# Kernel optimization log

Measured on AMD Instinct MI355X. Metric: run time of the kernel, lower is better.

The kernel has to match this reference:

```python
import jax, jax.numpy as jnp
import numpy as np

H, HID, VD, NB = 8, 128, 16, 4
EN_LOC, DE_LOC = 5.0, 5.0
FMAX = jnp.float32(3.4028235e38)

def _gelu(x):
    return jax.nn.gelu(x, approximate=False)  # keras gelu default = erf form

def _mlp(x, W1, b1, W2, b2):
    return _gelu(x @ W1 + b1) @ W2 + b2

def _mhpa(m_dist, x, r, w, locality):
    # m_dist: (B,N,N), r: (1,H,1,1), w: (H,HID,VD)
    sd = m_dist[:, None, :, :] * (r ** 2)  # (B,H,N,N)
    if locality <= 100:
        n = sd.shape[-1]
        pos = locality / 100.0 * (n - 1)  # tfp linear percentile position
        lo = int(np.floor(pos)); hi = int(np.ceil(pos)); frac = np.float32(pos - lo)
        s = jnp.sort(sd, axis=-1)
        thr = s[..., lo] * (1.0 - frac) + s[..., hi] * frac  # (B,H,N)
        sd = jnp.where(sd <= thr[..., None], sd, FMAX)
    att = jax.nn.softmax(-sd, axis=-1)  # masked entries -> exp(-huge) = 0
    v = jnp.einsum('bnj,hjk->bhnk', x, w)  # (B,H,N,VD)
    o = jnp.einsum('bhnj,bhjd->bhnd', att, v)  # (B,H,N,VD)
    B, Hh, N, D = o.shape
    return _gelu(o.transpose(0, 2, 1, 3).reshape(B, N, Hh * D))

def setup_inputs() -> dict:
    B, N, IN, OUT = 2, 2048, 3, 1
    ks = jax.random.split(jax.random.key(0), 40)
    def dn(k, shape, fan):
        return (jax.random.normal(k, shape) / np.sqrt(fan)).astype(jnp.float32)
    d = {}
    d['m_dist'] = jax.random.uniform(ks[0], (B, N, N), dtype=jnp.float32)
    d['inputs'] = jax.random.normal(ks[1], (B, N, IN), dtype=jnp.float32)
    d['en_W'] = dn(ks[2], (IN, HID), IN); d['en_b'] = jnp.zeros((HID,), jnp.float32)
    d['down_r'] = jax.random.uniform(ks[3], (1, H, 1, 1), dtype=jnp.float32)
    d['down_w'] = dn(ks[4], (H, HID, VD), HID)
    d['mlp1_W1'] = dn(ks[5], (HID, HID), HID); d['mlp1_b1'] = jnp.zeros((HID,), jnp.float32)
    d['mlp1_W2'] = dn(ks[6], (HID, HID), HID); d['mlp1_b2'] = jnp.zeros((HID,), jnp.float32)
    d['w1_W'] = dn(ks[7], (HID, HID), HID); d['w1_b'] = jnp.zeros((HID,), jnp.float32)
    d['pa_r'] = jax.random.uniform(ks[8], (NB, 1, H, 1, 1), dtype=jnp.float32)
    d['pa_w'] = dn(ks[9], (NB, H, HID, VD), HID)
    d['blk_W1'] = dn(ks[10], (NB, HID, HID), HID); d['blk_b1'] = jnp.zeros((NB, HID), jnp.float32)
    d['blk_W2'] = dn(ks[11], (NB, HID, HID), HID); d['blk_b2'] = jnp.zeros((NB, HID), jnp.float32)
    d['wi_W'] = dn(ks[12], (NB, HID, HID), HID); d['wi_b'] = jnp.zeros((NB, HID), jnp.float32)
    d['up_r'] = jax.random.uniform(ks[13], (1, H, 1, 1), dtype=jnp.float32)
    d['up_w'] = dn(ks[14], (H, HID, VD), HID)
    d['mlp2_W1'] = dn(ks[15], (HID, HID), HID); d['mlp2_b1'] = jnp.zeros((HID,), jnp.float32)
    d['mlp2_W2'] = dn(ks[16], (HID, HID), HID); d['mlp2_b2'] = jnp.zeros((HID,), jnp.float32)
    d['w2_W'] = dn(ks[17], (HID, HID), HID); d['w2_b'] = jnp.zeros((HID,), jnp.float32)
    d['de_W1'] = dn(ks[18], (HID, HID), HID); d['de_b1'] = jnp.zeros((HID,), jnp.float32)
    d['de_W2'] = dn(ks[19], (HID, OUT), HID); d['de_b2'] = jnp.zeros((OUT,), jnp.float32)
    return d

def reference(m_dist, inputs, en_W, en_b, down_r, down_w, mlp1_W1, mlp1_b1, mlp1_W2, mlp1_b2,
              w1_W, w1_b, pa_r, pa_w, blk_W1, blk_b1, blk_W2, blk_b2, wi_W, wi_b,
              up_r, up_w, mlp2_W1, mlp2_b1, mlp2_W2, mlp2_b2, w2_W, w2_b,
              de_W1, de_b1, de_W2, de_b2):
    en = _gelu(inputs @ en_W + en_b)
    x = _mlp(_mhpa(m_dist, en, down_r, down_w, EN_LOC), mlp1_W1, mlp1_b1, mlp1_W2, mlp1_b2) + (en @ w1_W + w1_b)
    x = _gelu(x)
    for i in range(NB):
        h = _mhpa(m_dist, x, pa_r[i], pa_w[i], 200)  # locality=200 -> no mask
        x = _gelu(_mlp(h, blk_W1[i], blk_b1[i], blk_W2[i], blk_b2[i]) + (x @ wi_W[i] + wi_b[i]))
    de = _mlp(_mhpa(m_dist, x, up_r, up_w, DE_LOC), mlp2_W1, mlp2_b1, mlp2_W2, mlp2_b2) + (x @ w2_W + w2_b)
    de = _gelu(de)
    return _mlp(de, de_W1, de_b1, de_W2, de_b2)
```

## Files before the change

kernel.cpp:

```cpp
#include <hip/hip_runtime.h>
#include <hip/hip_bf16.h>
#include <cstddef>

#define NROWS 4096
#define HIDD  128
#define NH    8
#define VD    16

typedef __attribute__((ext_vector_type(8))) short bf16x8;
typedef __attribute__((ext_vector_type(4))) float f32x4;
typedef __attribute__((ext_vector_type(4))) unsigned int u32x4;

__device__ __forceinline__ float gelu_f(float x) {
    return 0.5f * x * (1.0f + erff(x * 0.70710678118654752440f));
}

__device__ __forceinline__ unsigned short bf16_rne(float f) {
    union { float f; unsigned u; } x; x.f = f;
    unsigned r = x.u + 0x7FFFu + ((x.u >> 16) & 1u);
    return (unsigned short)(r >> 16);
}
__device__ __forceinline__ float bf16_to_f(unsigned short h) {
    union { unsigned u; float f; } x; x.u = ((unsigned)h) << 16;
    return x.f;
}
__device__ __forceinline__ unsigned pk_bf16(float a, float b) {
    __hip_bfloat162 t = __float22bfloat162_rn(make_float2(a, b));
    unsigned u; __builtin_memcpy(&u, &t, 4); return u;
}

__device__ __forceinline__ void split8(const float* av, bf16x8& hi, bf16x8& lo) {
    #pragma unroll
    for (int j = 0; j < 8; ++j) {
        unsigned short h = bf16_rne(av[j]);
        unsigned short l = bf16_rne(av[j] - bf16_to_f(h));
        hi[j] = (short)h; lo[j] = (short)l;
    }
}

__device__ __forceinline__ void load_a_global(const float* __restrict__ X,
                                              int row0, int lane,
                                              bf16x8* ahi, bf16x8* alo) {
    const int q = lane >> 4, mr = lane & 15;
    const float* xr = X + (size_t)(row0 + mr) * 128 + q * 8;
    #pragma unroll
    for (int kt = 0; kt < 4; ++kt) {
        float av[8];
        *(float4*)(av)     = *(const float4*)(xr + kt * 32);
        *(float4*)(av + 4) = *(const float4*)(xr + kt * 32 + 4);
        split8(av, ahi[kt], alo[kt]);
    }
}
__device__ __forceinline__ void load_a_lds(const float (*xT)[132], int lane,
                                           bf16x8* ahi, bf16x8* alo) {
    const int q = lane >> 4, mr = lane & 15;
    #pragma unroll
    for (int kt = 0; kt < 4; ++kt) {
        float av[8];
        *(float4*)(av)     = *(const float4*)&xT[mr][kt * 32 + q * 8];
        *(float4*)(av + 4) = *(const float4*)&xT[mr][kt * 32 + q * 8 + 4];
        split8(av, ahi[kt], alo[kt]);
    }
}

__device__ __forceinline__ f32x4 mm3(f32x4 acc, bf16x8 ahi, bf16x8 alo,
                                     const unsigned short* __restrict__ bp, int kt) {
    bf16x8 bhi = *(const bf16x8*)(bp + kt * 512);
    bf16x8 blo = *(const bf16x8*)(bp + 16384 + kt * 512);
    acc = __builtin_amdgcn_mfma_f32_16x16x32_bf16(ahi, bhi, acc, 0, 0, 0);
    acc = __builtin_amdgcn_mfma_f32_16x16x32_bf16(ahi, blo, acc, 0, 0, 0);
    acc = __builtin_amdgcn_mfma_f32_16x16x32_bf16(alo, bhi, acc, 0, 0, 0);
    return acc;
}

__device__ __forceinline__ void vproj_lds(const float (*xT)[132], int row0,
                                          const unsigned short* __restrict__ Vw,
                                          unsigned short* __restrict__ vblk) {
    const int tid = threadIdx.x, wave = tid >> 6, lane = tid & 63;
    const int q = lane >> 4, mr = lane & 15;
    bf16x8 ahi[4], alo[4];
    load_a_lds(xT, lane, ahi, alo);
    #pragma unroll
    for (int ct = 0; ct < 2; ++ct) {
        int nt = wave * 2 + ct;
        const unsigned short* bp = Vw + (size_t)nt * 2048 + lane * 8;
        f32x4 acc = (f32x4){0.f, 0.f, 0.f, 0.f};
        #pragma unroll
        for (int kt = 0; kt < 4; ++kt) acc = mm3(acc, ahi[kt], alo[kt], bp, kt);
        int c = nt * 16 + mr;
        int r0 = row0 + q * 4;
        int bb = r0 >> 11, n = r0 & 2047;
        int jt = n >> 5, q2 = (n >> 3) & 3, jj = n & 7;
        int h = c >> 4, dd = c & 15;
        size_t off = (((size_t)(bb * 8 + h) * 64 + jt) * 4 + q2) * 128
                   + (dd << 3) + jj;
        uint2 st = make_uint2(pk_bf16(acc[0], acc[1]), pk_bf16(acc[2], acc[3]));
        *(uint2*)(vblk + off) = st;
    }
}

struct PrepArgs { const float* src[25]; unsigned vwmask; };

__global__ __launch_bounds__(256) void prep_percentile_kernel(
    PrepArgs a, unsigned short* __restrict__ dst,
    const float* __restrict__ m, float* __restrict__ m102, float* __restrict__ m103)
{
    if (blockIdx.x < 100) {
        const int mat = blockIdx.x >> 2, chunk = blockIdx.x & 3;
        const float* __restrict__ W = a.src[mat];
        const int vw = (a.vwmask >> mat) & 1;
        unsigned short* __restrict__ base = dst + (size_t)mat * 32768;
        for (int o = chunk * 4096 + threadIdx.x; o < chunk * 4096 + 4096; o += 256) {
            int nt = o >> 11, kt = (o >> 9) & 3, q = (o >> 7) & 3;
            int n16 = (o >> 3) & 15, jj = o & 7;
            int k = kt * 32 + q * 8 + jj;
            float w = vw ? W[nt * 2048 + k * 16 + n16]
                         : W[k * 128 + nt * 16 + n16];
            unsigned short h = bf16_rne(w);
            unsigned short l = bf16_rne(w - bf16_to_f(h));
            base[o] = h;
            base[16384 + o] = l;
        }
        return;
    }

    __shared__ int   cnt[256];
    __shared__ int   cum[256];
    __shared__ float buf[192];
    __shared__ int   nc;
    __shared__ int   sb0, sb1, sbase;

    const int row = blockIdx.x - 100;
    const int t   = threadIdx.x;
    const float* mr = m + (size_t)row * 2048;

    float4 aa = *(const float4*)(mr + t * 8);
    float4 cc = *(const float4*)(mr + t * 8 + 4);
    float v[8] = {aa.x, aa.y, aa.z, aa.w, cc.x, cc.y, cc.z, cc.w};

    cnt[t] = 0;
    if (t == 0) nc = 0;
    __syncthreads();

    int bidx[8];
    #pragma unroll
    for (int i = 0; i < 8; ++i) {
        int bi = (int)(v[i] * 256.0f);
        bi = bi < 0 ? 0 : (bi > 255 ? 255 : bi);
        bidx[i] = bi;
        atomicAdd(&cnt[bi], 1);
    }
    __syncthreads();

    if (t < 64) {
        int c0 = cnt[t * 4], c1 = cnt[t * 4 + 1], c2 = cnt[t * 4 + 2], c3 = cnt[t * 4 + 3];
        int s1 = c0 + c1, s2 = s1 + c2, s3 = s2 + c3;
        int sc = s3;
        #pragma unroll
        for (int off = 1; off < 64; off <<= 1) {
            int o = __shfl_up(sc, off);
            if (t >= off) sc += o;
        }
        int base = sc - s3;
        cum[t * 4]     = base + c0;
        cum[t * 4 + 1] = base + s1;
        cum[t * 4 + 2] = base + s2;
        cum[t * 4 + 3] = base + s3;
    }
    __syncthreads();

    {
        int cprev = (t == 0) ? 0 : cum[t - 1];
        int cthis = cum[t];
        if (cprev < 103 && 103 <= cthis) { sb0 = t; sbase = cprev; }
        if (cprev < 104 && 104 <= cthis) { sb1 = t; }
    }
    __syncthreads();

    const int b0 = sb0, b1 = sb1, base = sbase;
    #pragma unroll
    for (int i = 0; i < 8; ++i) {
        if (bidx[i] >= b0 && bidx[i] <= b1) {
            int p = atomicAdd(&nc, 1);
            if (p < 192) buf[p] = v[i];
        }
    }
    __syncthreads();

    int n = nc; if (n > 192) n = 192;
    if (t < n) {
        float x = buf[t];
        int rk = base;
        for (int j = 0; j < n; ++j) {
            float y = buf[j];
            rk += (y < x || (y == x && j < t)) ? 1 : 0;
        }
        if (rk == 102) m102[row] = x;
        if (rk == 103) m103[row] = x;
    }
}

__global__ __launch_bounds__(256) void encoder_vproj_kernel(
    const float* __restrict__ inp, const float* __restrict__ W,
    const float* __restrict__ b, float* __restrict__ ben,
    const unsigned short* __restrict__ Vw, unsigned short* __restrict__ vblk)
{
    __shared__ float xT[16][132];
    const int tid = threadIdx.x;
    const int row0 = blockIdx.x * 16;
    const int ri = tid >> 4, c0 = (tid & 15) * 8;
    const int row = row0 + ri;
    float x0 = inp[row * 3], x1 = inp[row * 3 + 1], x2 = inp[row * 3 + 2];
    float o[8];
    #pragma unroll
    for (int j = 0; j < 8; ++j) {
        int c = c0 + j;
        o[j] = gelu_f(x0 * W[c] + x1 * W[128 + c] + x2 * W[256 + c] + b[c]);
        xT[ri][c0 + j] = o[j];
    }
    *(float4*)(ben + (size_t)row * 128 + c0)     = *(float4*)(o);
    *(float4*)(ben + (size_t)row * 128 + c0 + 4) = *(float4*)(o + 4);
    __syncthreads();
    vproj_lds(xT, row0, Vw, vblk);
}

__global__ __launch_bounds__(512) void attn_mlp_kernel(
    const float* __restrict__ m_dist,
    const unsigned short* __restrict__ vblk,
    const float* __restrict__ rvec,
    const float* __restrict__ m102, const float* __restrict__ m103,
    const unsigned short* __restrict__ W1b, const float* __restrict__ b1,
    float* __restrict__ bt, int masked)
{
    __shared__ float partLDS[4][16][128];
    __shared__ float sumLDS[4][8][16];
    __shared__ float bhT[16][132];

    const int tid  = threadIdx.x;
    const int wave = tid >> 6, lane = tid & 63;
    const int hg = wave & 1, jq = wave >> 1;
    const int q = lane >> 4, rn = lane & 15;
    const int row0 = blockIdx.x * 16;
    const int row  = row0 + rn;
    const int b    = row0 >> 11;
    const int n    = row & 2047;

    float r2[4], c2[4], thr[4];
    {
        const double pos = 5.0 / 100.0 * 2047.0;
        const float FRAC = (float)(pos - 102.0);
        const float OM   = 1.0f - FRAC;
        float t102 = m102[row], t103 = m103[row];
        #pragma unroll
        for (int hh = 0; hh < 4; ++hh) {
            float r = rvec[hg * 4 + hh];
            r2[hh] = r * r;
            c2[hh] = -r2[hh] * 1.44269504088896340736f;
            thr[hh] = masked ? ((t102 * r2[hh]) * OM + (t103 * r2[hh]) * FRAC)
                             : 3.4028235e38f;
        }
    }

    const float* mrow = m_dist + ((size_t)b << 22) + ((size_t)n << 11);
    const unsigned short* vbase = vblk + (((size_t)(b * 8 + hg * 4)) << 15);

    f32x4 acc[4], accs[4];
    #pragma unroll
    for (int hh = 0; hh < 4; ++hh) {
        acc[hh]  = (f32x4){0.f, 0.f, 0.f, 0.f};
        accs[hh] = (f32x4){0.f, 0.f, 0.f, 0.f};
    }
    bf16x8 vones;
    #pragma unroll
    for (int j = 0; j < 8; ++j) vones[j] = (short)0x3F80;

    const int jbeg = jq * 16, jend = jbeg + 16;

    float mvA[8], mvB[8]; bf16x8 bfA[4], bfB[4];

    auto loadjt = [&](int jt, float* mv, bf16x8* bf) {
        const int jb = (jt << 5) + (q << 3);
        *(float4*)(mv)     = *(const float4*)(mrow + jb);
        *(float4*)(mv + 4) = *(const float4*)(mrow + jb + 4);
        #pragma unroll
        for (int hh = 0; hh < 4; ++hh)
            bf[hh] = *(const bf16x8*)(vbase + ((size_t)hh << 15)
                                       + ((size_t)jt << 9) + (lane << 3));
    };
    auto compute = [&](const float* mv, const bf16x8* bf) {
        #pragma unroll
        for (int hh = 0; hh < 4; ++hh) {
            float p[8];
            if (masked) {
                #pragma unroll
                for (int jj = 0; jj < 8; ++jj) {
                    float sd = mv[jj] * r2[hh];
                    float e  = __builtin_amdgcn_exp2f(mv[jj] * c2[hh]);
                    p[jj] = (sd <= thr[hh]) ? e : 0.f;
                }
            } else {
                #pragma unroll
                for (int jj = 0; jj < 8; ++jj)
                    p[jj] = __builtin_amdgcn_exp2f(mv[jj] * c2[hh]);
            }
            u32x4 af;
            af[0] = pk_bf16(p[0], p[1]); af[1] = pk_bf16(p[2], p[3]);
            af[2] = pk_bf16(p[4], p[5]); af[3] = pk_bf16(p[6], p[7]);
            bf16x8 afrag = __builtin_bit_cast(bf16x8, af);
            acc[hh]  = __builtin_amdgcn_mfma_f32_16x16x32_bf16(afrag, bf[hh], acc[hh], 0, 0, 0);
            accs[hh] = __builtin_amdgcn_mfma_f32_16x16x32_bf16(afrag, vones,  accs[hh], 0, 0, 0);
        }
    };

    loadjt(jbeg, mvA, bfA);
    for (int jt = jbeg; jt < jend; jt += 2) {
        loadjt(jt + 1, mvB, bfB);
        compute(mvA, bfA);
        int j2 = (jt + 2 < jend) ? jt + 2 : jend - 1;
        loadjt(j2, mvA, bfA);
        compute(mvB, bfB);
    }

    if (rn == 0) {
        #pragma unroll
        for (int hh = 0; hh < 4; ++hh)
            #pragma unroll
            for (int reg = 0; reg < 4; ++reg)
                sumLDS[jq][hg * 4 + hh][q * 4 + reg] = accs[hh][reg];
    }
    #pragma unroll
    for (int hh = 0; hh < 4; ++hh) {
        #pragma unroll
        for (int reg = 0; reg < 4; ++reg)
            partLDS[jq][q * 4 + reg][(hg * 4 + hh) * 16 + rn] = acc[hh][reg];
    }
    __syncthreads();

    {
        int e0 = tid << 2;
        int ri = e0 >> 7, c0e = e0 & 127, h = c0e >> 4;
        float4 s = *(const float4*)&partLDS[0][ri][c0e];
        #pragma unroll
        for (int k = 1; k < 4; ++k) {
            float4 pz = *(const float4*)&partLDS[k][ri][c0e];
            s.x += pz.x; s.y += pz.y; s.z += pz.z; s.w += pz.w;
        }
        float l = sumLDS[0][h][ri] + sumLDS[1][h][ri]
                + sumLDS[2][h][ri] + sumLDS[3][h][ri];
        float inv = 1.0f / l;
        float4 o;
        o.x = gelu_f(s.x * inv); o.y = gelu_f(s.y * inv);
        o.z = gelu_f(s.z * inv); o.w = gelu_f(s.w * inv);
        *(float4*)&bhT[ri][c0e] = o;
    }
    __syncthreads();

    {
        bf16x8 ahi[4], alo[4];
        load_a_lds(bhT, lane, ahi, alo);
        const unsigned short* bp = W1b + (size_t)wave * 2048 + lane * 8;
        f32x4 a2 = (f32x4){0.f, 0.f, 0.f, 0.f};
        #pragma unroll
        for (int kt = 0; kt < 4; ++kt) a2 = mm3(a2, ahi[kt], alo[kt], bp, kt);
        const int c = wave * 16 + rn;
        const float bv = b1[c];
        #pragma unroll
        for (int reg = 0; reg < 4; ++reg)
            bt[(size_t)(row0 + q * 4 + reg) * 128 + c] = gelu_f(a2[reg] + bv);
    }
}

__global__ __launch_bounds__(256) void mm2_vproj_kernel(
    const float* __restrict__ A1, const unsigned short* __restrict__ B1,
    const float* __restrict__ bias1,
    const float* __restrict__ A2, const unsigned short* __restrict__ B2,
    const float* __restrict__ bias2,
    float* __restrict__ xout,
    const unsigned short* __restrict__ Vw, unsigned short* __restrict__ vblk)
{
    __shared__ float xT[16][132];
    const int tid = threadIdx.x, wave = tid >> 6, lane = tid & 63;
    const int q = lane >> 4, mr = lane & 15;
    const int row0 = blockIdx.x * 16;

    bf16x8 a1h[4], a1l[4], a2h[4], a2l[4];
    load_a_global(A1, row0, lane, a1h, a1l);
    load_a_global(A2, row0, lane, a2h, a2l);

    #pragma unroll
    for (int ct = 0; ct < 2; ++ct) {
        int nt = wave * 2 + ct;
        const unsigned short* bp1 = B1 + (size_t)nt * 2048 + lane * 8;
        const unsigned short* bp2 = B2 + (size_t)nt * 2048 + lane * 8;
        f32x4 acc = (f32x4){0.f, 0.f, 0.f, 0.f};
        #pragma unroll
        for (int kt = 0; kt < 4; ++kt) acc = mm3(acc, a1h[kt], a1l[kt], bp1, kt);
        #pragma unroll
        for (int kt = 0; kt < 4; ++kt) acc = mm3(acc, a2h[kt], a2l[kt], bp2, kt);
        int c = nt * 16 + mr;
        float bv = bias1[c] + bias2[c];
        #pragma unroll
        for (int reg = 0; reg < 4; ++reg) {
            float v = gelu_f(acc[reg] + bv);
            xout[(size_t)(row0 + q * 4 + reg) * 128 + c] = v;
            xT[q * 4 + reg][c] = v;
        }
    }
    __syncthreads();
    vproj_lds(xT, row0, Vw, vblk);
}

__global__ __launch_bounds__(256) void mm2_decoder_kernel(
    const float* __restrict__ A1, const unsigned short* __restrict__ B1,
    const float* __restrict__ bias1,
    const float* __restrict__ A2, const unsigned short* __restrict__ B2,
    const float* __restrict__ bias2,
    const unsigned short* __restrict__ DW1, const float* __restrict__ db1,
    const float* __restrict__ de_W2, const float* __restrict__ de_b2,
    float* __restrict__ out)
{
    __shared__ float xT[16][132];
    __shared__ float tT[16][132];
    const int tid = threadIdx.x, wave = tid >> 6, lane = tid & 63;
    const int q = lane >> 4, mr = lane & 15;
    const int row0 = blockIdx.x * 16;

    bf16x8 a1h[4], a1l[4], a2h[4], a2l[4];
    load_a_global(A1, row0, lane, a1h, a1l);
    load_a_global(A2, row0, lane, a2h, a2l);

    #pragma unroll
    for (int ct = 0; ct < 2; ++ct) {
        int nt = wave * 2 + ct;
        const unsigned short* bp1 = B1 + (size_t)nt * 2048 + lane * 8;
        const unsigned short* bp2 = B2 + (size_t)nt * 2048 + lane * 8;
        f32x4 acc = (f32x4){0.f, 0.f, 0.f, 0.f};
        #pragma unroll
        for (int kt = 0; kt < 4; ++kt) acc = mm3(acc, a1h[kt], a1l[kt], bp1, kt);
        #pragma unroll
        for (int kt = 0; kt < 4; ++kt) acc = mm3(acc, a2h[kt], a2l[kt], bp2, kt);
        int c = nt * 16 + mr;
        float bv = bias1[c] + bias2[c];
        #pragma unroll
        for (int reg = 0; reg < 4; ++reg)
            xT[q * 4 + reg][c] = gelu_f(acc[reg] + bv);
    }
    __syncthreads();

    {
        bf16x8 ahi[4], alo[4];
        load_a_lds(xT, lane, ahi, alo);
        #pragma unroll
        for (int ct = 0; ct < 2; ++ct) {
            int nt = wave * 2 + ct;
            const unsigned short* bp = DW1 + (size_t)nt * 2048 + lane * 8;
            f32x4 acc = (f32x4){0.f, 0.f, 0.f, 0.f};
            #pragma unroll
            for (int kt = 0; kt < 4; ++kt) acc = mm3(acc, ahi[kt], alo[kt], bp, kt);
            int c = nt * 16 + mr;
            #pragma unroll
            for (int reg = 0; reg < 4; ++reg)
                tT[q * 4 + reg][c] = gelu_f(acc[reg] + db1[c]);
        }
    }
    __syncthreads();

    {
        int r = tid >> 4, ch = tid & 15;
        const float* tp = &tT[r][ch * 8];
        const float* wp = de_W2 + ch * 8;
        float p = 0.f;
        #pragma unroll
        for (int j = 0; j < 8; ++j) p += tp[j] * wp[j];
        p += __shfl_xor(p, 1); p += __shfl_xor(p, 2);
        p += __shfl_xor(p, 4); p += __shfl_xor(p, 8);
        if (ch == 0) out[row0 + r] = p + de_b2[0];
    }
}

extern "C" void kernel_launch(void* const* d_in, const int* in_sizes, int n_in,
                              void* d_out, int out_size, void* d_ws, size_t ws_size,
                              hipStream_t stream)
{
    (void)in_sizes; (void)n_in; (void)out_size; (void)ws_size;
    const float* m_dist  = (const float*)d_in[0];
    const float* inputs  = (const float*)d_in[1];
    const float* en_W    = (const float*)d_in[2];
    const float* en_b    = (const float*)d_in[3];
    const float* down_r  = (const float*)d_in[4];
    const float* down_w  = (const float*)d_in[5];
    const float* mlp1_W1 = (const float*)d_in[6];
    const float* mlp1_b1 = (const float*)d_in[7];
    const float* mlp1_W2 = (const float*)d_in[8];
    const float* mlp1_b2 = (const float*)d_in[9];
    const float* w1_W    = (const float*)d_in[10];
    const float* w1_b    = (const float*)d_in[11];
    const float* pa_r    = (const float*)d_in[12];
    const float* pa_w    = (const float*)d_in[13];
    const float* blk_W1  = (const float*)d_in[14];
    const float* blk_b1  = (const float*)d_in[15];
    const float* blk_W2  = (const float*)d_in[16];
    const float* blk_b2  = (const float*)d_in[17];
    const float* wi_W    = (const float*)d_in[18];
    const float* wi_b    = (const float*)d_in[19];
    const float* up_r    = (const float*)d_in[20];
    const float* up_w    = (const float*)d_in[21];
    const float* mlp2_W1 = (const float*)d_in[22];
    const float* mlp2_b1 = (const float*)d_in[23];
    const float* mlp2_W2 = (const float*)d_in[24];
    const float* mlp2_b2 = (const float*)d_in[25];
    const float* w2_W    = (const float*)d_in[26];
    const float* w2_b    = (const float*)d_in[27];
    const float* de_W1   = (const float*)d_in[28];
    const float* de_b1   = (const float*)d_in[29];
    const float* de_W2   = (const float*)d_in[30];
    const float* de_b2   = (const float*)d_in[31];
    float* out = (float*)d_out;

    const size_t BUF = (size_t)NROWS * HIDD;
    float* w     = (float*)d_ws;
    float* ben   = w;
    float* bx0   = w + 1 * BUF;
    float* bx1   = w + 2 * BUF;
    float* bt    = w + 3 * BUF;
    unsigned short* vblk = (unsigned short*)(w + 4 * BUF);
    float* m102  = w + 5 * BUF;
    float* m103  = m102 + NROWS;
    unsigned short* wcvt = (unsigned short*)(m103 + NROWS);

    enum { CW_DOWN = 0, CW_MLP1W1 = 1, CW_MLP1W2 = 2, CW_W1 = 3,
           CW_PA = 4 , CW_BLKW1 = 8, CW_BLKW2 = 12, CW_WI = 16,
           CW_UP = 20, CW_MLP2W1 = 21, CW_MLP2W2 = 22, CW_W2 = 23, CW_DE1 = 24 };
    PrepArgs pa;
    pa.src[CW_DOWN]   = down_w;
    pa.src[CW_MLP1W1] = mlp1_W1;
    pa.src[CW_MLP1W2] = mlp1_W2;
    pa.src[CW_W1]     = w1_W;
    for (int i = 0; i < 4; ++i) {
        pa.src[CW_PA + i]    = pa_w   + (size_t)i * NH * HIDD * VD;
        pa.src[CW_BLKW1 + i] = blk_W1 + (size_t)i * HIDD * HIDD;
        pa.src[CW_BLKW2 + i] = blk_W2 + (size_t)i * HIDD * HIDD;
        pa.src[CW_WI + i]    = wi_W   + (size_t)i * HIDD * HIDD;
    }
    pa.src[CW_UP]     = up_w;
    pa.src[CW_MLP2W1] = mlp2_W1;
    pa.src[CW_MLP2W2] = mlp2_W2;
    pa.src[CW_W2]     = w2_W;
    pa.src[CW_DE1]    = de_W1;
    pa.vwmask = (1u << CW_DOWN) | (0xFu << CW_PA) | (1u << CW_UP);

    auto CW = [&](int slot) { return wcvt + (size_t)slot * 32768; };

    dim3 b256(256), b512(512);
    dim3 gT(NROWS / 16);

    auto K1 = [&](const float* rv, int masked, int w1slot, const float* b1v) {
        attn_mlp_kernel<<<gT, b512, 0, stream>>>(m_dist, vblk, rv, m102, m103,
                                                 CW(w1slot), b1v, bt, masked);
    };
    auto K2 = [&](int s1, const float* bias1, const float* A2, int s2,
                  const float* bias2, float* xo, int vslot) {
        mm2_vproj_kernel<<<gT, b256, 0, stream>>>(bt, CW(s1), bias1,
                                                  A2, CW(s2), bias2,
                                                  xo, CW(vslot), vblk);
    };

    prep_percentile_kernel<<<dim3(100 + NROWS), b256, 0, stream>>>(
        pa, wcvt, m_dist, m102, m103);

    encoder_vproj_kernel<<<gT, b256, 0, stream>>>(inputs, en_W, en_b, ben,
                                                  CW(CW_DOWN), vblk);

    K1(down_r, 1, CW_MLP1W1, mlp1_b1);
    K2(CW_MLP1W2, mlp1_b2, ben, CW_W1, w1_b, bx0, CW_PA + 0);

    float* xin = bx0;
    float* xout = bx1;
    for (int i = 0; i < 4; ++i) {
        K1(pa_r + (size_t)i * NH, 0, CW_BLKW1 + i, blk_b1 + (size_t)i * HIDD);
        K2(CW_BLKW2 + i, blk_b2 + (size_t)i * HIDD,
           xin, CW_WI + i, wi_b + (size_t)i * HIDD,
           xout, (i < 3) ? (CW_PA + i + 1) : CW_UP);
        float* tmp = xin; xin = xout; xout = tmp;
    }

    K1(up_r, 1, CW_MLP2W1, mlp2_b1);
    mm2_decoder_kernel<<<gT, b256, 0, stream>>>(
        bt, CW(CW_MLP2W2), mlp2_b2,
        xin, CW(CW_W2), w2_b,
        CW(CW_DE1), de_b1, de_W2, de_b2, out);
}
```

Baseline: 316.2 us.

## Fuse attention, MLP, residual matmul and V-projection into one stage kernel

Merges the attention+first-MLP kernel with the following mm2+vproj kernel (and the decoder kernel) into a single 512-thread kernel per stage, keeping intermediate bt tiles in LDS instead of global memory. V blocks are double-buffered (vblkA/vblkB) since a stage now reads the previous V while writing the next. This removes six kernel launches and the bt round-trip, at the cost of higher LDS use per block and each wave handling one output column tile instead of two.

```diff
diff --git a/kernel.cpp b/kernel.cpp
--- a/kernel.cpp
+++ b/kernel.cpp
@@ -97,6 +97,73 @@
         uint2 st = make_uint2(pk_bf16(acc[0], acc[1]), pk_bf16(acc[2], acc[3]));
         *(uint2*)(vblk + off) = st;
     }
+}
+
+
+__device__ __forceinline__ void mm_lds_tile(const float (*src)[132], float (*dst)[132],
+                                            const unsigned short* __restrict__ Wb,
+                                            const float* __restrict__ bias,
+                                            int wave, int lane) {
+    bf16x8 ahi[4], alo[4];
+    load_a_lds(src, lane, ahi, alo);
+    const unsigned short* bp = Wb + (size_t)wave * 2048 + lane * 8;
+    f32x4 acc = (f32x4){0.f, 0.f, 0.f, 0.f};
+    #pragma unroll
+    for (int kt = 0; kt < 4; ++kt) acc = mm3(acc, ahi[kt], alo[kt], bp, kt);
+    const int q = lane >> 4, rn = lane & 15, c = wave * 16 + rn;
+    const float bv = bias[c];
+    #pragma unroll
+    for (int reg = 0; reg < 4; ++reg)
+        dst[q * 4 + reg][c] = gelu_f(acc[reg] + bv);
+}
+
+__device__ __forceinline__ void mm2_tile(const float (*A1)[132],
+                                         const float* __restrict__ A2, int row0,
+                                         const unsigned short* __restrict__ B1,
+                                         const float* __restrict__ bias1,
+                                         const unsigned short* __restrict__ B2,
+                                         const float* __restrict__ bias2,
+                                         float* __restrict__ xout, float (*xT)[132],
+                                         int wave, int lane) {
+    bf16x8 a1h[4], a1l[4], a2h[4], a2l[4];
+    load_a_lds(A1, lane, a1h, a1l);
+    load_a_global(A2, row0, lane, a2h, a2l);
+    const unsigned short* bp1 = B1 + (size_t)wave * 2048 + lane * 8;
+    const unsigned short* bp2 = B2 + (size_t)wave * 2048 + lane * 8;
+    f32x4 acc = (f32x4){0.f, 0.f, 0.f, 0.f};
+    #pragma unroll
+    for (int kt = 0; kt < 4; ++kt) acc = mm3(acc, a1h[kt], a1l[kt], bp1, kt);
+    #pragma unroll
+    for (int kt = 0; kt < 4; ++kt) acc = mm3(acc, a2h[kt], a2l[kt], bp2, kt);
+    const int q = lane >> 4, rn = lane & 15, c = wave * 16 + rn;
+    const float bv = bias1[c] + bias2[c];
+    #pragma unroll
+    for (int reg = 0; reg < 4; ++reg) {
+        float v = gelu_f(acc[reg] + bv);
+        if (xout) xout[(size_t)(row0 + q * 4 + reg) * 128 + c] = v;
+        xT[q * 4 + reg][c] = v;
+    }
+}
+
+__device__ __forceinline__ void vproj8(const float (*xT)[132], int row0,
+                                       const unsigned short* __restrict__ Vw,
+                                       unsigned short* __restrict__ vout,
+                                       int wave, int lane) {
+    bf16x8 ahi[4], alo[4];
+    load_a_lds(xT, lane, ahi, alo);
+    const unsigned short* bp = Vw + (size_t)wave * 2048 + lane * 8;
+    f32x4 acc = (f32x4){0.f, 0.f, 0.f, 0.f};
+    #pragma unroll
+    for (int kt = 0; kt < 4; ++kt) acc = mm3(acc, ahi[kt], alo[kt], bp, kt);
+    const int q = lane >> 4, mr = lane & 15, c = wave * 16 + mr;
+    int r0 = row0 + q * 4;
+    int bb = r0 >> 11, n = r0 & 2047;
+    int jt = n >> 5, q2 = (n >> 3) & 3, jj = n & 7;
+    int h = c >> 4, dd = c & 15;
+    size_t off = (((size_t)(bb * 8 + h) * 64 + jt) * 4 + q2) * 128
+               + (dd << 3) + jj;
+    uint2 st = make_uint2(pk_bf16(acc[0], acc[1]), pk_bf16(acc[2], acc[3]));
+    *(uint2*)(vout + off) = st;
 }
 
 struct PrepArgs { const float* src[25]; unsigned vwmask; };
@@ -224,23 +291,17 @@
     vproj_lds(xT, row0, Vw, vblk);
 }
 
-__global__ __launch_bounds__(512) void attn_mlp_kernel(
-    const float* __restrict__ m_dist,
-    const unsigned short* __restrict__ vblk,
+__device__ __forceinline__ void attn_stage(
+    const float* __restrict__ m_dist, const unsigned short* __restrict__ vblk,
     const float* __restrict__ rvec,
     const float* __restrict__ m102, const float* __restrict__ m103,
-    const unsigned short* __restrict__ W1b, const float* __restrict__ b1,
-    float* __restrict__ bt, int masked)
+    int masked, int row0,
+    float (*partLDS)[16][128], float (*sumLDS)[8][16], float (*bhT)[132])
 {
-    __shared__ float partLDS[4][16][128];
-    __shared__ float sumLDS[4][8][16];
-    __shared__ float bhT[16][132];
-
     const int tid  = threadIdx.x;
     const int wave = tid >> 6, lane = tid & 63;
     const int hg = wave & 1, jq = wave >> 1;
     const int q = lane >> 4, rn = lane & 15;
-    const int row0 = blockIdx.x * 16;
     const int row  = row0 + rn;
     const int b    = row0 >> 11;
     const int n    = row & 2047;
@@ -354,118 +415,76 @@
         *(float4*)&bhT[ri][c0e] = o;
     }
     __syncthreads();
-
-    {
-        bf16x8 ahi[4], alo[4];
-        load_a_lds(bhT, lane, ahi, alo);
-        const unsigned short* bp = W1b + (size_t)wave * 2048 + lane * 8;
-        f32x4 a2 = (f32x4){0.f, 0.f, 0.f, 0.f};
-        #pragma unroll
-        for (int kt = 0; kt < 4; ++kt) a2 = mm3(a2, ahi[kt], alo[kt], bp, kt);
-        const int c = wave * 16 + rn;
-        const float bv = b1[c];
-        #pragma unroll
-        for (int reg = 0; reg < 4; ++reg)
-            bt[(size_t)(row0 + q * 4 + reg) * 128 + c] = gelu_f(a2[reg] + bv);
-    }
-}
-
-__global__ __launch_bounds__(256) void mm2_vproj_kernel(
-    const float* __restrict__ A1, const unsigned short* __restrict__ B1,
-    const float* __restrict__ bias1,
-    const float* __restrict__ A2, const unsigned short* __restrict__ B2,
-    const float* __restrict__ bias2,
+}
+
+__global__ __launch_bounds__(512) void stage_kernel(
+    const float* __restrict__ m_dist, const unsigned short* __restrict__ vin,
+    const float* __restrict__ rvec,
+    const float* __restrict__ m102, const float* __restrict__ m103,
+    const unsigned short* __restrict__ W1b, const float* __restrict__ b1,
+    const unsigned short* __restrict__ W2b, const float* __restrict__ b2,
+    const float* __restrict__ xin, const unsigned short* __restrict__ Wib,
+    const float* __restrict__ bi,
     float* __restrict__ xout,
-    const unsigned short* __restrict__ Vw, unsigned short* __restrict__ vblk)
+    const unsigned short* __restrict__ Vw, unsigned short* __restrict__ vout,
+    int masked)
 {
+    __shared__ float partLDS[4][16][128];
+    __shared__ float sumLDS[4][8][16];
+    __shared__ float bhT[16][132];
+    __shared__ float btT[16][132];
     __shared__ float xT[16][132];
+
     const int tid = threadIdx.x, wave = tid >> 6, lane = tid & 63;
-    const int q = lane >> 4, mr = lane & 15;
     const int row0 = blockIdx.x * 16;
 
-    bf16x8 a1h[4], a1l[4], a2h[4], a2l[4];
-    load_a_global(A1, row0, lane, a1h, a1l);
-    load_a_global(A2, row0, lane, a2h, a2l);
-
-    #pragma unroll
-    for (int ct = 0; ct < 2; ++ct) {
-        int nt = wave * 2 + ct;
-        const unsigned short* bp1 = B1 + (size_t)nt * 2048 + lane * 8;
-        const unsigned short* bp2 = B2 + (size_t)nt * 2048 + lane * 8;
-        f32x4 acc = (f32x4){0.f, 0.f, 0.f, 0.f};
-        #pragma unroll
-        for (int kt = 0; kt < 4; ++kt) acc = mm3(acc, a1h[kt], a1l[kt], bp1, kt);
-        #pragma unroll
-        for (int kt = 0; kt < 4; ++kt) acc = mm3(acc, a2h[kt], a2l[kt], bp2, kt);
-        int c = nt * 16 + mr;
-        float bv = bias1[c] + bias2[c];
-        #pragma unroll
-        for (int reg = 0; reg < 4; ++reg) {
-            float v = gelu_f(acc[reg] + bv);
-            xout[(size_t)(row0 + q * 4 + reg) * 128 + c] = v;
-            xT[q * 4 + reg][c] = v;
-        }
-    }
-    __syncthreads();
-    vproj_lds(xT, row0, Vw, vblk);
-}
-
-__global__ __launch_bounds__(256) void mm2_decoder_kernel(
-    const float* __restrict__ A1, const unsigned short* __restrict__ B1,
-    const float* __restrict__ bias1,
-    const float* __restrict__ A2, const unsigned short* __restrict__ B2,
-    const float* __restrict__ bias2,
+    attn_stage(m_dist, vin, rvec, m102, m103, masked, row0,
+               partLDS, sumLDS, bhT);
+
+    mm_lds_tile(bhT, btT, W1b, b1, wave, lane);
+    __syncthreads();
+
+    mm2_tile(btT, xin, row0, W2b, b2, Wib, bi, xout, xT, wave, lane);
+    __syncthreads();
+
+    vproj8(xT, row0, Vw, vout, wave, lane);
+}
+
+__global__ __launch_bounds__(512) void decoder_stage_kernel(
+    const float* __restrict__ m_dist, const unsigned short* __restrict__ vin,
+    const float* __restrict__ rvec,
+    const float* __restrict__ m102, const float* __restrict__ m103,
+    const unsigned short* __restrict__ W1b, const float* __restrict__ b1,
+    const unsigned short* __restrict__ W2b, const float* __restrict__ b2,
+    const float* __restrict__ xin, const unsigned short* __restrict__ Wib,
+    const float* __restrict__ bi,
     const unsigned short* __restrict__ DW1, const float* __restrict__ db1,
     const float* __restrict__ de_W2, const float* __restrict__ de_b2,
     float* __restrict__ out)
 {
+    __shared__ float partLDS[4][16][128];
+    __shared__ float sumLDS[4][8][16];
+    __shared__ float bhT[16][132];
+    __shared__ float btT[16][132];
     __shared__ float xT[16][132];
     __shared__ float tT[16][132];
+
     const int tid = threadIdx.x, wave = tid >> 6, lane = tid & 63;
-    const int q = lane >> 4, mr = lane & 15;
     const int row0 = blockIdx.x * 16;
 
-    bf16x8 a1h[4], a1l[4], a2h[4], a2l[4];
-    load_a_global(A1, row0, lane, a1h, a1l);
-    load_a_global(A2, row0, lane, a2h, a2l);
-
-    #pragma unroll
-    for (int ct = 0; ct < 2; ++ct) {
-        int nt = wave * 2 + ct;
-        const unsigned short* bp1 = B1 + (size_t)nt * 2048 + lane * 8;
-        const unsigned short* bp2 = B2 + (size_t)nt * 2048 + lane * 8;
-        f32x4 acc = (f32x4){0.f, 0.f, 0.f, 0.f};
-        #pragma unroll
-        for (int kt = 0; kt < 4; ++kt) acc = mm3(acc, a1h[kt], a1l[kt], bp1, kt);
-        #pragma unroll
-        for (int kt = 0; kt < 4; ++kt) acc = mm3(acc, a2h[kt], a2l[kt], bp2, kt);
-        int c = nt * 16 + mr;
-        float bv = bias1[c] + bias2[c];
-        #pragma unroll
-        for (int reg = 0; reg < 4; ++reg)
-            xT[q * 4 + reg][c] = gelu_f(acc[reg] + bv);
-    }
-    __syncthreads();
-
-    {
-        bf16x8 ahi[4], alo[4];
-        load_a_lds(xT, lane, ahi, alo);
-        #pragma unroll
-        for (int ct = 0; ct < 2; ++ct) {
-            int nt = wave * 2 + ct;
-            const unsigned short* bp = DW1 + (size_t)nt * 2048 + lane * 8;
-            f32x4 acc = (f32x4){0.f, 0.f, 0.f, 0.f};
-            #pragma unroll
-            for (int kt = 0; kt < 4; ++kt) acc = mm3(acc, ahi[kt], alo[kt], bp, kt);
-            int c = nt * 16 + mr;
-            #pragma unroll
-            for (int reg = 0; reg < 4; ++reg)
-                tT[q * 4 + reg][c] = gelu_f(acc[reg] + db1[c]);
-        }
-    }
-    __syncthreads();
-
-    {
+    attn_stage(m_dist, vin, rvec, m102, m103, 1, row0,
+               partLDS, sumLDS, bhT);
+
+    mm_lds_tile(bhT, btT, W1b, b1, wave, lane);
+    __syncthreads();
+
+    mm2_tile(btT, xin, row0, W2b, b2, Wib, bi, nullptr, xT, wave, lane);
+    __syncthreads();
+
+    mm_lds_tile(xT, tT, DW1, db1, wave, lane);
+    __syncthreads();
+
+    if (tid < 256) {
         int r = tid >> 4, ch = tid & 15;
         const float* tp = &tT[r][ch * 8];
         const float* wp = de_W2 + ch * 8;
@@ -522,9 +541,9 @@
     float* ben   = w;
     float* bx0   = w + 1 * BUF;
     float* bx1   = w + 2 * BUF;
-    float* bt    = w + 3 * BUF;
-    unsigned short* vblk = (unsigned short*)(w + 4 * BUF);
-    float* m102  = w + 5 * BUF;
+    unsigned short* vblkA = (unsigned short*)(w + 3 * BUF);
+    unsigned short* vblkB = (unsigned short*)(w + 3 * BUF + BUF / 2);
+    float* m102  = w + 4 * BUF;
     float* m103  = m102 + NROWS;
     unsigned short* wcvt = (unsigned short*)(m103 + NROWS);
 
@@ -554,39 +573,35 @@
     dim3 b256(256), b512(512);
     dim3 gT(NROWS / 16);
 
-    auto K1 = [&](const float* rv, int masked, int w1slot, const float* b1v) {
-        attn_mlp_kernel<<<gT, b512, 0, stream>>>(m_dist, vblk, rv, m102, m103,
-                                                 CW(w1slot), b1v, bt, masked);
-    };
-    auto K2 = [&](int s1, const float* bias1, const float* A2, int s2,
-                  const float* bias2, float* xo, int vslot) {
-        mm2_vproj_kernel<<<gT, b256, 0, stream>>>(bt, CW(s1), bias1,
-                                                  A2, CW(s2), bias2,
-                                                  xo, CW(vslot), vblk);
-    };
-
     prep_percentile_kernel<<<dim3(100 + NROWS), b256, 0, stream>>>(
         pa, wcvt, m_dist, m102, m103);
 
     encoder_vproj_kernel<<<gT, b256, 0, stream>>>(inputs, en_W, en_b, ben,
-                                                  CW(CW_DOWN), vblk);
-
-    K1(down_r, 1, CW_MLP1W1, mlp1_b1);
-    K2(CW_MLP1W2, mlp1_b2, ben, CW_W1, w1_b, bx0, CW_PA + 0);
+                                                  CW(CW_DOWN), vblkA);
+
+    stage_kernel<<<gT, b512, 0, stream>>>(
+        m_dist, vblkA, down_r, m102, m103,
+        CW(CW_MLP1W1), mlp1_b1, CW(CW_MLP1W2), mlp1_b2,
+        ben, CW(CW_W1), w1_b, bx0, CW(CW_PA + 0), vblkB, 1);
 
     float* xin = bx0;
     float* xout = bx1;
+    unsigned short* vin = vblkB;
+    unsigned short* vou = vblkA;
     for (int i = 0; i < 4; ++i) {
-        K1(pa_r + (size_t)i * NH, 0, CW_BLKW1 + i, blk_b1 + (size_t)i * HIDD);
-        K2(CW_BLKW2 + i, blk_b2 + (size_t)i * HIDD,
-           xin, CW_WI + i, wi_b + (size_t)i * HIDD,
-           xout, (i < 3) ? (CW_PA + i + 1) : CW_UP);
-        float* tmp = xin; xin = xout; xout = tmp;
-    }
-
-    K1(up_r, 1, CW_MLP2W1, mlp2_b1);
-    mm2_decoder_kernel<<<gT, b256, 0, stream>>>(
-        bt, CW(CW_MLP2W2), mlp2_b2,
+        stage_kernel<<<gT, b512, 0, stream>>>(
+            m_dist, vin, pa_r + (size_t)i * NH, m102, m103,
+            CW(CW_BLKW1 + i), blk_b1 + (size_t)i * HIDD,
+            CW(CW_BLKW2 + i), blk_b2 + (size_t)i * HIDD,
+            xin, CW(CW_WI + i), wi_b + (size_t)i * HIDD,
+            xout, (i < 3) ? CW(CW_PA + i + 1) : CW(CW_UP), vou, 0);
+        float* t = xin; xin = xout; xout = t;
+        unsigned short* tv = vin; vin = vou; vou = tv;
+    }
+
+    decoder_stage_kernel<<<gT, b512, 0, stream>>>(
+        m_dist, vin, up_r, m102, m103,
+        CW(CW_MLP2W1), mlp2_b1, CW(CW_MLP2W2), mlp2_b2,
         xin, CW(CW_W2), w2_b,
         CW(CW_DE1), de_b1, de_W2, de_b2, out);
 }
```

After: 289.9 us. -8.3%, faster.
